# Kernel tuning notes

Measured on AMD Instinct MI355X. Metric: run time of the kernel, lower is better.

## Reference

```python
import jax, jax.numpy as jnp
import numpy as np

D_MODEL = 1024
NHEAD = 16
D_K = D_MODEL // NHEAD


def setup_inputs() -> dict:
    key = jax.random.key(0)
    ks = jax.random.split(key, 10)
    B, S = 2, 2048
    x = jax.random.normal(ks[0], (B, S, D_MODEL), dtype=jnp.float32)
    # sorted 1-D coordinate grid in [0,1], shape [S,1,1] so coords.shape[1]==1
    coords = jnp.sort(jax.random.uniform(ks[1], (S, 1, 1), dtype=jnp.float32), axis=0)
    sc = 1.0 / np.sqrt(D_MODEL)
    Wq = jax.random.normal(ks[2], (D_MODEL, D_MODEL), dtype=jnp.float32) * sc
    bq = jnp.zeros((D_MODEL,), jnp.float32)
    Wk = jax.random.normal(ks[3], (D_MODEL, D_MODEL), dtype=jnp.float32) * sc
    bk = jnp.zeros((D_MODEL,), jnp.float32)
    Wv = jax.random.normal(ks[4], (D_MODEL, D_MODEL), dtype=jnp.float32) * sc
    bv = jnp.zeros((D_MODEL,), jnp.float32)
    Wo = jax.random.normal(ks[5], (D_MODEL, D_MODEL), dtype=jnp.float32) * sc
    bo = jnp.zeros((D_MODEL,), jnp.float32)
    return {"x": x, "coords": coords, "Wq": Wq, "bq": bq, "Wk": Wk, "bk": bk,
            "Wv": Wv, "bv": bv, "Wo": Wo, "bo": bo}


def _split_heads(t):  # [B,S,D] -> [B,H,S,Dk]
    B, S, _ = t.shape
    return t.reshape(B, S, NHEAD, D_K).transpose(0, 2, 1, 3)


def reference(x, coords, Wq, bq, Wk, bk, Wv, bv, Wo, bo):
    B, S, _ = x.shape
    Q = _split_heads(x @ Wq.T + bq)
    K = _split_heads(x @ Wk.T + bk)
    V = _split_heads(x @ Wv.T + bv)

    scale = jnp.sqrt(jnp.float32(D_K))
    scores = jnp.einsum('bhld,bhsd->bhls', Q, K) / scale  # [B,H,S,S]

    # trapezoidal quadrature weights from coord grid: [S-1] -> broadcast shapes
    dc = jnp.abs(coords[1:] - coords[:-1]).reshape(1, 1, 1, S - 1)  # key-axis

    # custom trapezoidal softmax
    e = jnp.exp(scores - jnp.max(scores, axis=-1, keepdims=True))
    denom = jnp.sum(0.5 * dc * (e[..., 1:] + e[..., :-1]), axis=-1, keepdims=True)
    aw = e / denom  # [B,H,S,S]

    dcv = dc.reshape(1, 1, S - 1, 1)  # value-axis weighting
    o1 = jnp.einsum('bhls,bhsd->bhld', aw[..., 1:], dcv * V[:, :, 1:, :])
    o2 = jnp.einsum('bhls,bhsd->bhld', aw[..., :-1], dcv * V[:, :, :-1, :])
    out = 0.5 * (o1 + o2)  # [B,H,S,Dk]

    out = out.transpose(0, 2, 1, 3).reshape(B, S, D_MODEL)
    return out @ Wo.T + bo
```

## Files before the change

kernel.cpp:

```cpp
#include <hip/hip_runtime.h>

#define DM 1024
#define NHEAD 16
#define DK 64
#define QLD 3072

typedef short bf16x8 __attribute__((ext_vector_type(8)));
typedef float f32x4 __attribute__((ext_vector_type(4)));

__device__ __forceinline__ unsigned short f2bf(float f) {
  union { float f; unsigned u; } v; v.f = f;
  return (unsigned short)((v.u + 0x7fffu + ((v.u >> 16) & 1u)) >> 16);
}
__device__ __forceinline__ float bf2f(unsigned short h) {
  union { unsigned u; float f; } v; v.u = ((unsigned)h) << 16; return v.f;
}
__device__ __forceinline__ float fexp2(float x) {
  float r; asm("v_exp_f32 %0, %1" : "=v"(r) : "v"(x)); return r;
}

__device__ __forceinline__ void gld16(const void* g, void* l) {
  __builtin_amdgcn_global_load_lds((const __attribute__((address_space(1))) void*)g,
                                   (__attribute__((address_space(3))) void*)l, 16, 0, 0);
}

__device__ __forceinline__ int kappa(int p) {
  return (p & 32) + (((p & 7) >> 2) << 4) + (((p >> 3) & 3) << 2) + (p & 3);
}

__global__ void k_prep(const float* __restrict__ x, const float* __restrict__ Wq,
                       const float* __restrict__ Wk, const float* __restrict__ Wv,
                       const float* __restrict__ Wo, const float* __restrict__ bq,
                       const float* __restrict__ bk, const float* __restrict__ bv,
                       const float* __restrict__ coords,
                       unsigned short* __restrict__ xb, unsigned short* __restrict__ Wcat,
                       unsigned short* __restrict__ Wob, float* __restrict__ bcat,
                       float* __restrict__ tw, unsigned short* __restrict__ twb,
                       int M, int S, float QS) {
  const int nx = M * DM / 4;
  const int nw = DM * DM / 4;
  const int total = nx + 4 * nw;
  int gid = blockIdx.x * 256 + threadIdx.x;

  auto conv4 = [&](const float* src, unsigned short* dst, int idx, float sc) {
    float4 v = *(const float4*)(src + idx * 4);
    ushort4 o;
    o.x = f2bf(v.x * sc); o.y = f2bf(v.y * sc);
    o.z = f2bf(v.z * sc); o.w = f2bf(v.w * sc);
    *(ushort4*)(dst + idx * 4) = o;
  };

  if (gid < nx) { conv4(x, xb, gid, 1.0f); return; }
  if (gid < nx + nw) { conv4(Wq, Wcat, gid - nx, QS); return; }
  if (gid < nx + 2 * nw) { conv4(Wk, Wcat + DM * DM, gid - nx - nw, 1.0f); return; }
  if (gid < nx + 3 * nw) { conv4(Wv, Wcat + 2 * DM * DM, gid - nx - 2 * nw, 1.0f); return; }
  if (gid < total) { conv4(Wo, Wob, gid - nx - 3 * nw, 1.0f); return; }

  int r = gid - total;
  if (r < 3 * DM) {
    float v = (r < DM) ? bq[r] * QS : (r < 2 * DM ? bk[r - DM] : bv[r - 2 * DM]);
    bcat[r] = v;
    return;
  }
  r -= 3 * DM;
  if (r < S) {
    auto twval = [&](int k) {
      float a = (k > 0)     ? fabsf(coords[k] - coords[k - 1]) : 0.f;
      float b = (k < S - 1) ? fabsf(coords[k + 1] - coords[k]) : 0.f;
      return 0.5f * (a + b);
    };
    tw[r] = twval(r);
    int key = (r & ~63) + kappa(r & 63);
    twb[r] = f2bf(twval(key));
  }
}

#define BM 128
#define BN 128
#define BKK 64

template<int OUTF32>
__global__ __launch_bounds__(256)
void gemm_bt(const unsigned short* __restrict__ A, const unsigned short* __restrict__ B,
             const float* __restrict__ bias, void* __restrict__ C,
             int M, int N, int K, int ldc) {
  __shared__ __align__(16) unsigned short smem[4][BM * BKK];
  const int tid = threadIdx.x;
  const int lane = tid & 63;
  const int wid = tid >> 6;
  const int rr = lane & 15, g = lane >> 4;
  const int nbn = N / BN;
  const int cpx = gridDim.x >> 3;
  const int bid = ((gridDim.x & 7) == 0) ? (blockIdx.x & 7) * cpx + (blockIdx.x >> 3)
                                         : blockIdx.x;
  const int bm = bid / nbn, bn = bid % nbn;
  const int wr = wid >> 1, wc = wid & 1;
  const int nkt = K / BKK;

  const unsigned short* Abase = A + (size_t)bm * BM * K;
  const unsigned short* Bbase = B + (size_t)bn * BN * K;

  auto stage = [&](int buf, int kt) {
#pragma unroll
    for (int j = 0; j < 4; ++j) {
      int o = j * 256 + tid;
      int row = o >> 3;
      int cb = ((o & 7) * 16) ^ ((row & 7) << 4);
      gld16((const char*)(Abase + (size_t)row * K + kt * BKK) + cb, &smem[buf][o * 8]);
      gld16((const char*)(Bbase + (size_t)row * K + kt * BKK) + cb, &smem[2 + buf][o * 8]);
    }
  };

  f32x4 acc[4][4] = {};
  stage(0, 0);
  int cur = 0;
  const int sw = (rr & 7) << 4;
  for (int kt = 0; kt < nkt; ++kt) {
    __syncthreads();
    if (kt + 1 < nkt) stage(cur ^ 1, kt + 1);
    const char* a0 = (const char*)&smem[cur][(wr * 64) * BKK];
    const char* b0 = (const char*)&smem[2 + cur][(wc * 64) * BKK];
#pragma unroll
    for (int kk = 0; kk < 2; ++kk) {
      const int co = (kk * 64 + g * 16);
      bf16x8 af[4], bfr[4];
#pragma unroll
      for (int m = 0; m < 4; ++m)
        af[m] = *(const bf16x8*)(a0 + (m * 16 + rr) * 128 + (co ^ sw));
#pragma unroll
      for (int n = 0; n < 4; ++n)
        bfr[n] = *(const bf16x8*)(b0 + (n * 16 + rr) * 128 + (co ^ sw));
      __builtin_amdgcn_s_setprio(1);
#pragma unroll
      for (int m = 0; m < 4; ++m)
#pragma unroll
        for (int n = 0; n < 4; ++n)
          acc[m][n] = __builtin_amdgcn_mfma_f32_16x16x32_bf16(af[m], bfr[n], acc[m][n], 0, 0, 0);
      __builtin_amdgcn_s_setprio(0);
    }
    cur ^= 1;
  }

  const int crow0 = bm * BM + wr * 64;
  const int ccol0 = bn * BN + wc * 64;
  if (OUTF32) {
#pragma unroll
    for (int n = 0; n < 4; ++n) {
      const int col = ccol0 + n * 16 + rr;
      const float bn_ = bias ? bias[col] : 0.f;
#pragma unroll
      for (int m = 0; m < 4; ++m)
#pragma unroll
        for (int r = 0; r < 4; ++r) {
          const int row = crow0 + m * 16 + g * 4 + r;
          ((float*)C)[(size_t)row * ldc + col] = acc[m][n][r] + bn_;
        }
    }
  } else {
    unsigned short* L = &smem[0][0];
    __syncthreads();
#pragma unroll
    for (int n = 0; n < 4; ++n) {
      const float bn_ = bias ? bias[ccol0 + n * 16 + rr] : 0.f;
#pragma unroll
      for (int m = 0; m < 4; ++m)
#pragma unroll
        for (int r = 0; r < 4; ++r)
          L[(wr * 64 + m * 16 + g * 4 + r) * 136 + wc * 64 + n * 16 + rr] =
              f2bf(acc[m][n][r] + bn_);
    }
    __syncthreads();
    unsigned short* Cb = (unsigned short*)C + (size_t)(bm * BM) * ldc + bn * BN;
#pragma unroll
    for (int i = 0; i < 8; ++i) {
      int o = i * 256 + tid;
      int row = o >> 4;
      int cc = (o & 15) * 8;
      uint4 v = *(const uint4*)&L[row * 136 + cc];
      *(uint4*)&Cb[(size_t)row * ldc + cc] = v;
    }
  }
}

__global__ __launch_bounds__(256)
void k_transpose(const unsigned short* __restrict__ V, const float* __restrict__ tw,
                 unsigned short* __restrict__ Vt, int S, int ld) {
  __shared__ __align__(16) unsigned short t[64][72];
  __shared__ float tws[64];
  const int nst = S / 64;
  int st = blockIdx.x % nst;
  int bh = blockIdx.x / nst;
  int h = bh & (NHEAD - 1), b = bh / NHEAD;
  const unsigned short* src = V + ((size_t)b * S + st * 64) * ld + h * DK;
  unsigned short* dst = Vt + (size_t)bh * DK * S + st * 64;
  int tid = threadIdx.x;
  if (tid < 64) tws[tid] = tw[st * 64 + tid];
#pragma unroll
  for (int i = 0; i < 2; ++i) {
    int r = i * 32 + (tid >> 3);
    int c = (tid & 7) * 8;
    *(uint4*)&t[r][c] = *(const uint4*)&src[(size_t)r * ld + c];
  }
  __syncthreads();
#pragma unroll
  for (int i = 0; i < 2; ++i) {
    int d = i * 32 + (tid >> 3);
    int p0 = (tid & 7) * 8;
    unsigned short tmp[8];
#pragma unroll
    for (int j = 0; j < 8; ++j) {
      int kl = kappa(p0 + j);
      tmp[j] = f2bf(bf2f(t[kl][d]) * tws[kl]);
    }
    *(uint4*)&dst[(size_t)d * S + p0] = *(const uint4*)&tmp[0];
  }
}

__global__ __launch_bounds__(256)
void k_attn(const unsigned short* __restrict__ QKV, const unsigned short* __restrict__ Vt,
            const unsigned short* __restrict__ twb, unsigned short* __restrict__ O, int S) {
  __shared__ __align__(16) unsigned short sK[2][128 * 64];
  __shared__ __align__(16) unsigned short sV[2][64 * 128];
  const int tid = threadIdx.x, lane = tid & 63, wid = tid >> 6;
  const int rr = lane & 15, g = lane >> 4;
  const int nqt = S / 128;
  const int cpx = gridDim.x >> 3;
  const int swz = (blockIdx.x & 7) * cpx + (blockIdx.x >> 3);
  const int qt = swz % nqt;
  const int bh = swz / nqt;
  const int h = bh & (NHEAD - 1), b = bh / NHEAD;

  const unsigned short* Qbase = QKV + ((size_t)b * S + qt * 128 + wid * 32) * QLD + h * DK;
  const unsigned short* Kbase = QKV + (size_t)b * S * QLD + DM + h * DK;
  const unsigned short* Vbase = Vt + (size_t)bh * DK * S;

  bf16x8 aq[2][2];
#pragma unroll
  for (int qm = 0; qm < 2; ++qm) {
    aq[qm][0] = *(const bf16x8*)&Qbase[(size_t)(qm * 16 + rr) * QLD + g * 8];
    aq[qm][1] = *(const bf16x8*)&Qbase[(size_t)(qm * 16 + rr) * QLD + 32 + g * 8];
  }

  f32x4 acc[2][5] = {};
  const f32x4 z0 = {};

  auto stage = [&](int buf, int kt) {
#pragma unroll
    for (int j = 0; j < 4; ++j) {
      int o = j * 256 + tid;
      int row = o >> 3;
      int cb = ((o & 7) * 16) ^ ((row & 7) << 4);
      gld16((const char*)(Kbase + (size_t)(kt * 128 + row) * QLD) + cb, &sK[buf][o * 8]);
    }
#pragma unroll
    for (int j = 0; j < 4; ++j) {
      int o = j * 256 + tid;
      int row = o >> 4;
      int cb = ((o & 15) * 16) ^ ((row & 7) << 4);
      gld16((const char*)(Vbase + (size_t)row * S + kt * 128) + cb, &sV[buf][o * 8]);
    }
  };

  stage(0, 0);
  int cur = 0;
  const int nkt = S / 128;
  const int swr = (rr & 7) << 4;
  for (int kt = 0; kt < nkt; ++kt) {
    __syncthreads();
    if (kt + 1 < nkt) stage(cur ^ 1, kt + 1);

    f32x4 s[2][2][4];
#pragma unroll
    for (int half = 0; half < 2; ++half) {
#pragma unroll
      for (int f = 0; f < 4; ++f) {
        const int row = half * 64 + f * 16 + rr;
        bf16x8 kA0 = *(const bf16x8*)((const char*)&sK[cur][row * 64] + ((g * 16) ^ swr));
        bf16x8 kA1 = *(const bf16x8*)((const char*)&sK[cur][row * 64] + ((64 + g * 16) ^ swr));
        __builtin_amdgcn_s_setprio(1);
#pragma unroll
        for (int qm = 0; qm < 2; ++qm) {
          f32x4 z = __builtin_amdgcn_mfma_f32_16x16x32_bf16(kA0, aq[qm][0], z0, 0, 0, 0);
          s[half][qm][f] = __builtin_amdgcn_mfma_f32_16x16x32_bf16(kA1, aq[qm][1], z, 0, 0, 0);
        }
        __builtin_amdgcn_s_setprio(0);
      }
    }

#pragma unroll
    for (int half = 0; half < 2; ++half)
#pragma unroll
      for (int qm = 0; qm < 2; ++qm)
#pragma unroll
        for (int f = 0; f < 4; ++f)
#pragma unroll
          for (int r = 0; r < 4; ++r)
            s[half][qm][f][r] = fexp2(s[half][qm][f][r]);

#pragma unroll
    for (int half = 0; half < 2; ++half) {
      bf16x8 pa[2][2];
#pragma unroll
      for (int qm = 0; qm < 2; ++qm)
#pragma unroll
        for (int kk = 0; kk < 2; ++kk) {
          union { bf16x8 v; unsigned u[4]; } pk;
          asm("v_cvt_pk_bf16_f32 %0, %1, %2" : "=v"(pk.u[0]) : "v"(s[half][qm][2*kk][0]),   "v"(s[half][qm][2*kk][1]));
          asm("v_cvt_pk_bf16_f32 %0, %1, %2" : "=v"(pk.u[1]) : "v"(s[half][qm][2*kk][2]),   "v"(s[half][qm][2*kk][3]));
          asm("v_cvt_pk_bf16_f32 %0, %1, %2" : "=v"(pk.u[2]) : "v"(s[half][qm][2*kk+1][0]), "v"(s[half][qm][2*kk+1][1]));
          asm("v_cvt_pk_bf16_f32 %0, %1, %2" : "=v"(pk.u[3]) : "v"(s[half][qm][2*kk+1][2]), "v"(s[half][qm][2*kk+1][3]));
          pa[qm][kk] = pk.v;
        }

      bf16x8 tw0 = *(const bf16x8*)&twb[kt * 128 + half * 64 + g * 8];
      bf16x8 tw1 = *(const bf16x8*)&twb[kt * 128 + half * 64 + 32 + g * 8];

#pragma unroll
      for (int kk = 0; kk < 2; ++kk) {
        __builtin_amdgcn_s_setprio(1);
#pragma unroll
        for (int n = 0; n < 4; ++n) {
          const int vrow = n * 16 + rr;
          const int cb = (half * 128 + kk * 64 + g * 16) ^ ((vrow & 7) << 4);
          bf16x8 bv = *(const bf16x8*)((const char*)&sV[cur][vrow * 128] + cb);
#pragma unroll
          for (int qm = 0; qm < 2; ++qm)
            acc[qm][n] = __builtin_amdgcn_mfma_f32_16x16x32_bf16(pa[qm][kk], bv, acc[qm][n], 0, 0, 0);
        }
#pragma unroll
        for (int qm = 0; qm < 2; ++qm)
          acc[qm][4] = __builtin_amdgcn_mfma_f32_16x16x32_bf16(pa[qm][kk], kk ? tw1 : tw0, acc[qm][4], 0, 0, 0);
        __builtin_amdgcn_s_setprio(0);
      }
    }
    cur ^= 1;
  }

  unsigned short* Ob = O + ((size_t)b * S + qt * 128 + wid * 32) * DM + h * DK;
#pragma unroll
  for (int qm = 0; qm < 2; ++qm)
#pragma unroll
    for (int n = 0; n < 4; ++n)
#pragma unroll
      for (int r = 0; r < 4; ++r) {
        const int q = qm * 16 + g * 4 + r;
        const int d = n * 16 + rr;
        Ob[(size_t)q * DM + d] = f2bf(acc[qm][n][r] / acc[qm][4][r]);
      }
}

extern "C" void kernel_launch(void* const* d_in, const int* in_sizes, int n_in,
                              void* d_out, int out_size, void* d_ws, size_t ws_size,
                              hipStream_t stream) {
  const float* x      = (const float*)d_in[0];
  const float* coords = (const float*)d_in[1];
  const float* Wq = (const float*)d_in[2];
  const float* bq = (const float*)d_in[3];
  const float* Wk = (const float*)d_in[4];
  const float* bk = (const float*)d_in[5];
  const float* Wv = (const float*)d_in[6];
  const float* bv = (const float*)d_in[7];
  const float* Wo = (const float*)d_in[8];
  const float* bo = (const float*)d_in[9];

  const int S = in_sizes[1];
  const int B = in_sizes[0] / (S * DM);
  const int M = B * S;
  const float QS = 0.18033688011112042f;

  char* w = (char*)d_ws;
  size_t off = 0;
  unsigned short* xb   = (unsigned short*)(w + off); off += (size_t)M * DM * 2;
  unsigned short* Wcat = (unsigned short*)(w + off); off += (size_t)3 * DM * DM * 2;
  unsigned short* Wob  = (unsigned short*)(w + off); off += (size_t)DM * DM * 2;
  unsigned short* QKVb = (unsigned short*)(w + off); off += (size_t)M * QLD * 2;
  unsigned short* Vtb  = (unsigned short*)(w + off); off += (size_t)M * DM * 2;
  float* tw  = (float*)(w + off); off += (size_t)S * 4;
  unsigned short* twb = (unsigned short*)(w + off); off += (size_t)S * 2;
  float* bcat = (float*)(w + off); off += (size_t)3 * DM * 4;
  unsigned short* Ob = xb;
  (void)ws_size; (void)n_in; (void)out_size;

  {
    int nx = M * DM / 4, nw = DM * DM / 4;
    int total = nx + 4 * nw;
    int tail = 3 * DM + S;
    int gridp = total / 256 + (tail + 255) / 256;
    k_prep<<<gridp, 256, 0, stream>>>(x, Wq, Wk, Wv, Wo, bq, bk, bv, coords,
                                      xb, Wcat, Wob, bcat, tw, twb, M, S, QS);
  }

  gemm_bt<0><<<(M / BM) * (3 * DM / BN), 256, 0, stream>>>(xb, Wcat, bcat, QKVb, M, 3 * DM, DM, QLD);

  k_transpose<<<B * NHEAD * (S / 64), 256, 0, stream>>>(QKVb + 2 * DM, tw, Vtb, S, QLD);
  k_attn<<<B * NHEAD * (S / 128), 256, 0, stream>>>(QKVb, Vtb, twb, Ob, S);

  gemm_bt<1><<<(M / BM) * (DM / BN), 256, 0, stream>>>(Ob, Wob, bo, d_out, M, DM, DM, DM);
}
```

Baseline: 113.1 us.

## Fuse V transpose and weighting into QKV GEMM epilogue, restructure attention score loop

The QKV projection GEMM now writes the V tiles directly into the transposed, quadrature-weighted, permuted Vt layout from its shared-memory epilogue, so the separate transpose kernel launch and its extra read of V are gone. The attention kernel also computes scores, exp and packing one half-tile at a time, which shrinks the live score register array. The fused epilogue writes Vt with a strided per-thread pattern and does scalar shared-memory reads, which may cost more than the old dedicated kernel. V columns are no longer stored to QKVb, which is safe only because attention reads V from Vt.

Measured after the change: 111.1 us. About the same (-1.8%).

```diff
diff --git a/kernel.cpp b/kernel.cpp
--- a/kernel.cpp
+++ b/kernel.cpp
@@ -79,11 +79,12 @@
 #define BN 128
 #define BKK 64
 
-template<int OUTF32>
+template<int OUTF32, int VFUSE>
 __global__ __launch_bounds__(256)
 void gemm_bt(const unsigned short* __restrict__ A, const unsigned short* __restrict__ B,
              const float* __restrict__ bias, void* __restrict__ C,
-             int M, int N, int K, int ldc) {
+             int M, int N, int K, int ldc,
+             const float* __restrict__ twp, unsigned short* __restrict__ Vt, int S) {
   __shared__ __align__(16) unsigned short smem[4][BM * BKK];
   const int tid = threadIdx.x;
   const int lane = tid & 63;
@@ -170,49 +171,39 @@
               f2bf(acc[m][n][r] + bn_);
     }
     __syncthreads();
-    unsigned short* Cb = (unsigned short*)C + (size_t)(bm * BM) * ldc + bn * BN;
-#pragma unroll
-    for (int i = 0; i < 8; ++i) {
-      int o = i * 256 + tid;
-      int row = o >> 4;
-      int cc = (o & 15) * 8;
-      uint4 v = *(const uint4*)&L[row * 136 + cc];
-      *(uint4*)&Cb[(size_t)row * ldc + cc] = v;
-    }
-  }
-}
-
-__global__ __launch_bounds__(256)
-void k_transpose(const unsigned short* __restrict__ V, const float* __restrict__ tw,
-                 unsigned short* __restrict__ Vt, int S, int ld) {
-  __shared__ __align__(16) unsigned short t[64][72];
-  __shared__ float tws[64];
-  const int nst = S / 64;
-  int st = blockIdx.x % nst;
-  int bh = blockIdx.x / nst;
-  int h = bh & (NHEAD - 1), b = bh / NHEAD;
-  const unsigned short* src = V + ((size_t)b * S + st * 64) * ld + h * DK;
-  unsigned short* dst = Vt + (size_t)bh * DK * S + st * 64;
-  int tid = threadIdx.x;
-  if (tid < 64) tws[tid] = tw[st * 64 + tid];
-#pragma unroll
-  for (int i = 0; i < 2; ++i) {
-    int r = i * 32 + (tid >> 3);
-    int c = (tid & 7) * 8;
-    *(uint4*)&t[r][c] = *(const uint4*)&src[(size_t)r * ld + c];
-  }
-  __syncthreads();
-#pragma unroll
-  for (int i = 0; i < 2; ++i) {
-    int d = i * 32 + (tid >> 3);
-    int p0 = (tid & 7) * 8;
-    unsigned short tmp[8];
-#pragma unroll
-    for (int j = 0; j < 8; ++j) {
-      int kl = kappa(p0 + j);
-      tmp[j] = f2bf(bf2f(t[kl][d]) * tws[kl]);
-    }
-    *(uint4*)&dst[(size_t)d * S + p0] = *(const uint4*)&tmp[0];
+    if (VFUSE && bn >= (2 * DM) / BN) {
+      const int tilesPerB = S / BM;
+      const int bb = bm / tilesPerB;
+      const int s0 = (bm % tilesPerB) * BM;
+      const int vcol0 = bn * BN - 2 * DM;
+      const int hh = tid >> 7;
+      const int dd = (tid >> 1) & 63;
+      const int stl = tid & 1;
+      const int head = (vcol0 >> 6) + hh;
+      const int lcol = hh * 64 + dd;
+      unsigned short* vdst = Vt + ((size_t)(bb * NHEAD + head) * DK + dd) * S + s0 + stl * 64;
+      const float* twg = twp + s0 + stl * 64;
+      unsigned short tmp[8];
+#pragma unroll
+      for (int j8 = 0; j8 < 8; ++j8) {
+#pragma unroll
+        for (int j = 0; j < 8; ++j) {
+          const int kl = kappa(j8 * 8 + j);
+          tmp[j] = f2bf(bf2f(L[(stl * 64 + kl) * 136 + lcol]) * twg[kl]);
+        }
+        *(uint4*)&vdst[j8 * 8] = *(const uint4*)&tmp[0];
+      }
+    } else {
+      unsigned short* Cb = (unsigned short*)C + (size_t)(bm * BM) * ldc + bn * BN;
+#pragma unroll
+      for (int i = 0; i < 8; ++i) {
+        int o = i * 256 + tid;
+        int row = o >> 4;
+        int cc = (o & 15) * 8;
+        uint4 v = *(const uint4*)&L[row * 136 + cc];
+        *(uint4*)&Cb[(size_t)row * ldc + cc] = v;
+      }
+    }
   }
 }
 
@@ -264,51 +255,46 @@
   stage(0, 0);
   int cur = 0;
   const int nkt = S / 128;
-  const int swr = (rr & 7) << 4;
   for (int kt = 0; kt < nkt; ++kt) {
     __syncthreads();
     if (kt + 1 < nkt) stage(cur ^ 1, kt + 1);
 
-    f32x4 s[2][2][4];
 #pragma unroll
     for (int half = 0; half < 2; ++half) {
+      f32x4 s[2][4];
 #pragma unroll
       for (int f = 0; f < 4; ++f) {
         const int row = half * 64 + f * 16 + rr;
+        const int swr = (rr & 7) << 4;
         bf16x8 kA0 = *(const bf16x8*)((const char*)&sK[cur][row * 64] + ((g * 16) ^ swr));
         bf16x8 kA1 = *(const bf16x8*)((const char*)&sK[cur][row * 64] + ((64 + g * 16) ^ swr));
         __builtin_amdgcn_s_setprio(1);
 #pragma unroll
         for (int qm = 0; qm < 2; ++qm) {
           f32x4 z = __builtin_amdgcn_mfma_f32_16x16x32_bf16(kA0, aq[qm][0], z0, 0, 0, 0);
-          s[half][qm][f] = __builtin_amdgcn_mfma_f32_16x16x32_bf16(kA1, aq[qm][1], z, 0, 0, 0);
+          s[qm][f] = __builtin_amdgcn_mfma_f32_16x16x32_bf16(kA1, aq[qm][1], z, 0, 0, 0);
         }
         __builtin_amdgcn_s_setprio(0);
       }
-    }
-
-#pragma unroll
-    for (int half = 0; half < 2; ++half)
+
 #pragma unroll
       for (int qm = 0; qm < 2; ++qm)
 #pragma unroll
         for (int f = 0; f < 4; ++f)
 #pragma unroll
           for (int r = 0; r < 4; ++r)
-            s[half][qm][f][r] = fexp2(s[half][qm][f][r]);
-
-#pragma unroll
-    for (int half = 0; half < 2; ++half) {
+            s[qm][f][r] = fexp2(s[qm][f][r]);
+
       bf16x8 pa[2][2];
 #pragma unroll
       for (int qm = 0; qm < 2; ++qm)
 #pragma unroll
         for (int kk = 0; kk < 2; ++kk) {
           union { bf16x8 v; unsigned u[4]; } pk;
-          asm("v_cvt_pk_bf16_f32 %0, %1, %2" : "=v"(pk.u[0]) : "v"(s[half][qm][2*kk][0]),   "v"(s[half][qm][2*kk][1]));
-          asm("v_cvt_pk_bf16_f32 %0, %1, %2" : "=v"(pk.u[1]) : "v"(s[half][qm][2*kk][2]),   "v"(s[half][qm][2*kk][3]));
-          asm("v_cvt_pk_bf16_f32 %0, %1, %2" : "=v"(pk.u[2]) : "v"(s[half][qm][2*kk+1][0]), "v"(s[half][qm][2*kk+1][1]));
-          asm("v_cvt_pk_bf16_f32 %0, %1, %2" : "=v"(pk.u[3]) : "v"(s[half][qm][2*kk+1][2]), "v"(s[half][qm][2*kk+1][3]));
+          asm("v_cvt_pk_bf16_f32 %0, %1, %2" : "=v"(pk.u[0]) : "v"(s[qm][2*kk][0]),   "v"(s[qm][2*kk][1]));
+          asm("v_cvt_pk_bf16_f32 %0, %1, %2" : "=v"(pk.u[1]) : "v"(s[qm][2*kk][2]),   "v"(s[qm][2*kk][3]));
+          asm("v_cvt_pk_bf16_f32 %0, %1, %2" : "=v"(pk.u[2]) : "v"(s[qm][2*kk+1][0]), "v"(s[qm][2*kk+1][1]));
+          asm("v_cvt_pk_bf16_f32 %0, %1, %2" : "=v"(pk.u[3]) : "v"(s[qm][2*kk+1][2]), "v"(s[qm][2*kk+1][3]));
           pa[qm][kk] = pk.v;
         }
 
@@ -390,10 +376,11 @@
                                       xb, Wcat, Wob, bcat, tw, twb, M, S, QS);
   }
 
-  gemm_bt<0><<<(M / BM) * (3 * DM / BN), 256, 0, stream>>>(xb, Wcat, bcat, QKVb, M, 3 * DM, DM, QLD);
-
-  k_transpose<<<B * NHEAD * (S / 64), 256, 0, stream>>>(QKVb + 2 * DM, tw, Vtb, S, QLD);
+  gemm_bt<0, 1><<<(M / BM) * (3 * DM / BN), 256, 0, stream>>>(
+      xb, Wcat, bcat, QKVb, M, 3 * DM, DM, QLD, tw, Vtb, S);
+
   k_attn<<<B * NHEAD * (S / 128), 256, 0, stream>>>(QKVb, Vtb, twb, Ob, S);
 
-  gemm_bt<1><<<(M / BM) * (DM / BN), 256, 0, stream>>>(Ob, Wob, bo, d_out, M, DM, DM, DM);
-}
+  gemm_bt<1, 0><<<(M / BM) * (DM / BN), 256, 0, stream>>>(
+      Ob, Wob, bo, d_out, M, DM, DM, DM, nullptr, nullptr, S);
+}
```
